# Optimization experiments

Hardware: AMD Instinct MI355X
Metric: run time of the kernel (lower is better)

## Reference

```python
import jax, jax.numpy as jnp
import numpy as np

RES0 = 128
SCALES = [1, 2, 4, 8]
OUT_DIM = 32
PLANES = [(0, 1), (0, 2), (1, 2)]  # itertools.combinations(range(3), 2)


def _bilinear(grid, cx, cy):
    """grid: [C,H,W]; cx maps to W, cy maps to H; coords in [-1,1].
    Matches F.grid_sample(mode='bilinear', align_corners=True, padding_mode='border')."""
    C, H, W = grid.shape
    x = jnp.clip((cx + 1.0) * 0.5 * (W - 1), 0.0, W - 1)
    y = jnp.clip((cy + 1.0) * 0.5 * (H - 1), 0.0, H - 1)
    x0 = jnp.floor(x)
    y0 = jnp.floor(y)
    wx = (x - x0)[:, None]  # [N,1]
    wy = (y - y0)[:, None]
    x0i = x0.astype(jnp.int32)
    y0i = y0.astype(jnp.int32)
    x1i = jnp.minimum(x0i + 1, W - 1)
    y1i = jnp.minimum(y0i + 1, H - 1)
    g00 = grid[:, y0i, x0i].T  # [N,C]
    g01 = grid[:, y0i, x1i].T
    g10 = grid[:, y1i, x0i].T
    g11 = grid[:, y1i, x1i].T
    top = g00 * (1.0 - wx) + g01 * wx
    bot = g10 * (1.0 - wx) + g11 * wx
    return top * (1.0 - wy) + bot * wy  # [N,C]


def _interpolate_ms_features(x, ms_grids):
    feats = []
    for scale_grids in ms_grids:  # fixed 4 scales
        interp_space = 1.0
        for ci, (a, b) in enumerate(PLANES):  # fixed 3 planes
            interp_space = interp_space * _bilinear(scale_grids[ci], x[:, a], x[:, b])
        feats.append(interp_space)
    return jnp.concatenate(feats, axis=-1)  # [N, 4*OUT_DIM]


def _mlp(f, w0, w1, w2):
    h = jax.nn.relu(f @ w0)
    h = jax.nn.relu(h @ w1)
    return h @ w2  # [N,1], linear output (tcnn, bias-free)


def setup_inputs() -> dict:
    key = jax.random.key(0)
    ks = jax.random.split(key, 16)
    N = 1_000_000
    inp = {"x": jax.random.uniform(ks[0], (N, 3), jnp.float32, -1.0, 1.0)}
    i = 1
    for s, mult in enumerate(SCALES):
        R = RES0 * mult
        for p in range(3):
            # nn.init.uniform_(a=0.1, b=0.5)
            inp[f"g{s}p{p}"] = jax.random.uniform(ks[i], (OUT_DIM, R, R), jnp.float32, 0.1, 0.5)
            i += 1
    F = OUT_DIM * len(SCALES)
    inp["w0"] = jax.random.normal(ks[13], (F, 64), jnp.float32) / np.sqrt(F).astype(np.float32)
    inp["w1"] = jax.random.normal(ks[14], (64, 64), jnp.float32) / 8.0
    inp["w2"] = jax.random.normal(ks[15], (64, 1), jnp.float32) / 8.0
    return inp


def reference(x, g0p0, g0p1, g0p2, g1p0, g1p1, g1p2, g2p0, g2p1, g2p2,
              g3p0, g3p1, g3p2, w0, w1, w2):
    ms_grids = [(g0p0, g0p1, g0p2), (g1p0, g1p1, g1p2),
                (g2p0, g2p1, g2p2), (g3p0, g3p1, g3p2)]
    features = _interpolate_ms_features(x, ms_grids)
    return _mlp(features, w0, w1, w2)
```

## Files before the change

kernel.cpp:

```cpp
#include <hip/hip_runtime.h>
#include <cstddef>


typedef unsigned short ushort_t;
typedef unsigned int uint_t;
typedef __bf16 bf16x8 __attribute__((ext_vector_type(8)));
typedef float f32x4 __attribute__((ext_vector_type(4)));

#define NBUCKET 32768

struct KParams {
  const float* x;
  const void* g[12];
  const float* w0;
  const float* w1;
  const float* w2;
  const ushort_t* w0T;
  const ushort_t* w1T;
  const float* xs;
  const int* sidx;
  float* out;
  int N;
};

struct TPA {
  const float* src[12];
  ushort_t* dst[12];
};

__device__ __forceinline__ ushort_t f32_to_bf16_rne(float f) {
  uint_t u = __float_as_uint(f);
  u = (u + 0x7FFFu + ((u >> 16) & 1u)) >> 16;
  return (ushort_t)u;
}

__global__ __launch_bounds__(256) void transpose_all(TPA tp) {
  const int b = blockIdx.x;
  int s, tile;
  if (b < 256) { s = 0; tile = b; }
  else if (b < 1280) { s = 1; tile = b - 256; }
  else if (b < 5376) { s = 2; tile = b - 1280; }
  else { s = 3; tile = b - 5376; }
  const int RR = 16384 << (2 * s);
  const int k = s * 3 + blockIdx.y;
  const float* __restrict__ in = tp.src[k];
  ushort_t* __restrict__ out = tp.dst[k];

  __shared__ float tile_s[32][65];
  const int p0 = tile * 64;
  {
    const int tp_ = threadIdx.x & 63;
    const int tc = threadIdx.x >> 6;
#pragma unroll
    for (int cc = 0; cc < 8; ++cc) {
      const int c = cc * 4 + tc;
      tile_s[c][tp_] = in[(size_t)c * RR + p0 + tp_];
    }
  }
  __syncthreads();
  {
    const int c2 = threadIdx.x & 15;
    const int tq = threadIdx.x >> 4;
    uint_t* o32 = (uint_t*)out;
#pragma unroll
    for (int pp = 0; pp < 4; ++pp) {
      const int pos = pp * 16 + tq;
      const uint_t lo = f32_to_bf16_rne(tile_s[2 * c2 + 0][pos]);
      const uint_t hi = f32_to_bf16_rne(tile_s[2 * c2 + 1][pos]);
      o32[(size_t)(p0 + pos) * 16 + c2] = lo | (hi << 16);
    }
  }
}

__global__ __launch_bounds__(256) void prep_weights(
    const float* __restrict__ w0, const float* __restrict__ w1,
    ushort_t* __restrict__ w0T, ushort_t* __restrict__ w1T) {
  const int t = threadIdx.x;
  for (int i = t; i < 128 * 64; i += 256) {
    const int k = i >> 6, n = i & 63;
    w0T[n * 128 + k] = f32_to_bf16_rne(w0[i]);
  }
  for (int i = t; i < 64 * 64; i += 256) {
    const int k = i >> 6, n = i & 63;
    w1T[n * 64 + k] = f32_to_bf16_rne(w1[i]);
  }
}

__device__ __forceinline__ uint_t spread5(uint_t v) {
  return (v & 1u) | ((v & 2u) << 2) | ((v & 4u) << 4) | ((v & 8u) << 6) |
         ((v & 16u) << 8);
}
__device__ __forceinline__ uint_t morton_key(const float* __restrict__ x,
                                             int i) {
  const float a = x[3 * i + 0];
  const float b = x[3 * i + 1];
  const float c = x[3 * i + 2];
  const uint_t ua = (uint_t)fminf(fmaxf((a + 1.0f) * 16.0f, 0.0f), 31.0f);
  const uint_t ub = (uint_t)fminf(fmaxf((b + 1.0f) * 16.0f, 0.0f), 31.0f);
  const uint_t uc = (uint_t)fminf(fmaxf((c + 1.0f) * 16.0f, 0.0f), 31.0f);
  return spread5(ua) | (spread5(ub) << 1) | (spread5(uc) << 2);
}

__global__ __launch_bounds__(256) void sort_hist(const float* __restrict__ x,
                                                 uint_t* __restrict__ cnt,
                                                 int N) {
  const int i = blockIdx.x * 256 + threadIdx.x;
  if (i < N) atomicAdd(&cnt[morton_key(x, i)], 1u);
}

__global__ __launch_bounds__(1024) void sort_scanA(uint_t* __restrict__ cnt,
                                                   uint_t* __restrict__ bsum) {
  __shared__ uint_t s[1024];
  const int t = threadIdx.x;
  const int idx = blockIdx.x * 1024 + t;
  const uint_t v = cnt[idx];
  s[t] = v;
  __syncthreads();
  for (int off = 1; off < 1024; off <<= 1) {
    uint_t u = 0;
    if (t >= off) u = s[t - off];
    __syncthreads();
    s[t] += u;
    __syncthreads();
  }
  cnt[idx] = s[t] - v;
  if (t == 1023) bsum[blockIdx.x] = s[t];
}

__global__ __launch_bounds__(256) void sort_scanB_prepw(
    uint_t* __restrict__ bsum, const float* __restrict__ w0,
    const float* __restrict__ w1, ushort_t* __restrict__ w0T,
    ushort_t* __restrict__ w1T) {
  const int t = threadIdx.x;
  if (t == 0) {
    uint_t run = 0;
#pragma unroll
    for (int i = 0; i < 32; ++i) {
      const uint_t c = bsum[i];
      bsum[i] = run;
      run += c;
    }
  }
  for (int i = t; i < 128 * 64; i += 256) {
    const int k = i >> 6, n = i & 63;
    w0T[n * 128 + k] = f32_to_bf16_rne(w0[i]);
  }
  for (int i = t; i < 64 * 64; i += 256) {
    const int k = i >> 6, n = i & 63;
    w1T[n * 64 + k] = f32_to_bf16_rne(w1[i]);
  }
}

__global__ __launch_bounds__(256) void sort_scatter(
    const float* __restrict__ x, uint_t* __restrict__ cnt,
    const uint_t* __restrict__ bsum, int* __restrict__ sidx,
    float* __restrict__ xs, int N) {
  const int i = blockIdx.x * 256 + threadIdx.x;
  if (i >= N) return;
  const uint_t key = morton_key(x, i);
  const uint_t pos = atomicAdd(&cnt[key], 1u) + bsum[key >> 10];
  sidx[pos] = i;
  xs[3 * pos + 0] = x[3 * i + 0];
  xs[3 * pos + 1] = x[3 * i + 1];
  xs[3 * pos + 2] = x[3 * i + 2];
}

template <bool SORTED>
__global__ __launch_bounds__(512, 8) void kplanes_fused_mfma(KParams P) {
  __shared__ float arena[8704];
  int4* o4s = (int4*)arena;
  float* wxs = arena + 3072;
  float* wys = arena + 3840;
  uint_t* feat32 = (uint_t*)(arena + 4608);
  float* px = arena + 4608;

  const int t = threadIdx.x;

  int bid = blockIdx.x;
  if (SORTED) {
    const int nblk = gridDim.x;
    const int q = nblk >> 3, r = nblk & 7;
    const int xcd = bid & 7, idx = bid >> 3;
    bid = (xcd < r ? xcd * (q + 1) : r * (q + 1) + (xcd - r) * q) + idx;
  }
  const int blk0 = bid * 64;

  if (SORTED) {
    if (t < 192) {
      int idx = blk0 * 3 + t;
      if (idx >= 3 * P.N) idx = 3 * P.N - 3 + (t % 3);
      px[t] = P.xs[idx];
    }
  } else {
    if (t < 192) {
      const int p = t / 3, e = t - p * 3;
      int Pi = blk0 + p;
      if (Pi >= P.N) Pi = P.N - 1;
      px[t] = P.x[3 * Pi + e];
    }
  }
  __syncthreads();

  for (int task = t; task < 768; task += 512) {
    const int pt = task & 63;
    const int sm = task >> 6;
    const int pl = sm >> 2;
    const int s = sm & 3;
    const float cx = (pl == 2) ? px[pt * 3 + 1] : px[pt * 3 + 0];
    const float cy = (pl == 0) ? px[pt * 3 + 1] : px[pt * 3 + 2];
    const int R = 128 << s;
    const float Rm1 = (float)(R - 1);
    const float u = fminf(fmaxf((cx + 1.0f) * 0.5f * Rm1, 0.0f), Rm1);
    const float v = fminf(fmaxf((cy + 1.0f) * 0.5f * Rm1, 0.0f), Rm1);
    const float fx0 = floorf(u), fy0 = floorf(v);
    const int x0 = (int)fx0, y0 = (int)fy0;
    const int x1 = min(x0 + 1, R - 1), y1 = min(y0 + 1, R - 1);
    int4 o4;
    o4.x = y0 * R + x0;
    o4.y = y0 * R + x1;
    o4.z = y1 * R + x0;
    o4.w = y1 * R + x1;
    o4s[task] = o4;
    wxs[task] = u - fx0;
    wys[task] = v - fy0;
  }
  __syncthreads();

  const int pt = t >> 3;
  const int q = t & 7;
  const int cg = q & 3;
  const int sh = q >> 2;
  uint_t* prow = feat32 + pt * 64;
  const int wxor = (pt & 7) << 2;

#define LOADP(gp, o, QA, QB, QC, QD)                              \
  QA = *(const uint4*)((gp) + (size_t)(o).x * 32 + cg * 8);       \
  QB = *(const uint4*)((gp) + (size_t)(o).y * 32 + cg * 8);       \
  QC = *(const uint4*)((gp) + (size_t)(o).z * 32 + cg * 8);       \
  QD = *(const uint4*)((gp) + (size_t)(o).w * 32 + cg * 8);

#define CH2(dA, dB, dC, dD, i0, i1)                                \
  {                                                                \
    float rl = __uint_as_float((dD) << 16) * w11;                  \
    rl = fmaf(__uint_as_float((dC) << 16), w10, rl);               \
    rl = fmaf(__uint_as_float((dB) << 16), w01, rl);               \
    rl = fmaf(__uint_as_float((dA) << 16), w00, rl);               \
    f[i0] *= rl;                                                   \
    float rh = __uint_as_float((dD)&0xFFFF0000u) * w11;            \
    rh = fmaf(__uint_as_float((dC)&0xFFFF0000u), w10, rh);         \
    rh = fmaf(__uint_as_float((dB)&0xFFFF0000u), w01, rh);         \
    rh = fmaf(__uint_as_float((dA)&0xFFFF0000u), w00, rh);         \
    f[i1] *= rh;                                                   \
  }

#define CONSUME(QA, QB, QC, QD, WX, WY)                            \
  {                                                                \
    const float w11 = (WX) * (WY);                                 \
    const float w10 = (WY)-w11;                                    \
    const float w01 = (WX)-w11;                                    \
    const float w00 = 1.0f - (WX)-w10;                             \
    CH2(QA.x, QB.x, QC.x, QD.x, 0, 1)                              \
    CH2(QA.y, QB.y, QC.y, QD.y, 2, 3)                              \
    CH2(QA.z, QB.z, QC.z, QD.z, 4, 5)                              \
    CH2(QA.w, QB.w, QC.w, QD.w, 6, 7)                              \
  }

#pragma unroll
  for (int j = 0; j < 2; ++j) {
    const int s = 2 * j + sh;
    const int b0 = s * 64 + pt;
    const int b1 = (4 + s) * 64 + pt;
    const int b2 = (8 + s) * 64 + pt;
    const int4 o0 = o4s[b0];
    const int4 o1 = o4s[b1];
    const int4 o2 = o4s[b2];
    const float wx0 = wxs[b0], wy0 = wys[b0];
    const float wx1 = wxs[b1], wy1 = wys[b1];
    const float wx2 = wxs[b2], wy2 = wys[b2];
    const ushort_t* g0 = (const ushort_t*)P.g[s * 3 + 0];
    const ushort_t* g1 = (const ushort_t*)P.g[s * 3 + 1];
    const ushort_t* g2 = (const ushort_t*)P.g[s * 3 + 2];

    uint4 A0, B0, C0, D0, A1, B1, C1, D1, A2, B2, C2, D2;
    LOADP(g0, o0, A0, B0, C0, D0)
    LOADP(g1, o1, A1, B1, C1, D1)
    float f[8] = {1.f, 1.f, 1.f, 1.f, 1.f, 1.f, 1.f, 1.f};
    CONSUME(A0, B0, C0, D0, wx0, wy0)
    LOADP(g2, o2, A2, B2, C2, D2)
    CONSUME(A1, B1, C1, D1, wx1, wy1)
    CONSUME(A2, B2, C2, D2, wx2, wy2)

    uint_t d0, d1, d2, d3;
    asm("v_cvt_pk_bf16_f32 %0, %1, %2" : "=v"(d0) : "v"(f[0]), "v"(f[1]));
    asm("v_cvt_pk_bf16_f32 %0, %1, %2" : "=v"(d1) : "v"(f[2]), "v"(f[3]));
    asm("v_cvt_pk_bf16_f32 %0, %1, %2" : "=v"(d2) : "v"(f[4]), "v"(f[5]));
    asm("v_cvt_pk_bf16_f32 %0, %1, %2" : "=v"(d3) : "v"(f[6]), "v"(f[7]));
    uint4 dv;
    dv.x = d0; dv.y = d1; dv.z = d2; dv.w = d3;
    *(uint4*)(prow + ((s * 16 + cg * 4) ^ wxor)) = dv;
  }
#undef LOADP
#undef CH2
#undef CONSUME
  __syncthreads();

  ushort_t* lds_h = (ushort_t*)arena;
  float(*oparts)[64] = (float(*)[64])(arena + 2048);

  const int w = __builtin_amdgcn_readfirstlane(t >> 6);
  const int mt = w & 3;
  const int nt0 = (w >> 2) << 1;
  const int ln = t & 15;
  const int lq = (t >> 4) & 3;
  const int arow = mt * 16 + ln;

  const uint_t* farow = feat32 + arow * 64;
  const int axor = (arow & 7) << 2;
  f32x4 acc0a = {0.f, 0.f, 0.f, 0.f}, acc0b = {0.f, 0.f, 0.f, 0.f};
  const ushort_t* w0a = P.w0T + (nt0 * 16 + ln) * 128 + lq * 8;
  const ushort_t* w0b = w0a + 16 * 128;
#pragma unroll
  for (int kt = 0; kt < 4; ++kt) {
    const bf16x8 aF = *(const bf16x8*)(farow + ((kt * 16 + lq * 4) ^ axor));
    const bf16x8 bFa = *(const bf16x8*)(w0a + kt * 32);
    const bf16x8 bFb = *(const bf16x8*)(w0b + kt * 32);
    acc0a = __builtin_amdgcn_mfma_f32_16x16x32_bf16(aF, bFa, acc0a, 0, 0, 0);
    acc0b = __builtin_amdgcn_mfma_f32_16x16x32_bf16(aF, bFb, acc0b, 0, 0, 0);
  }

#pragma unroll
  for (int i = 0; i < 2; ++i) {
    const f32x4 a = i ? acc0b : acc0a;
    const int col = (nt0 + i) * 16 + ln;
#pragma unroll
    for (int jj = 0; jj < 4; ++jj) {
      const float v = fmaxf(a[jj], 0.0f);
      uint_t dv;
      asm("v_cvt_pk_bf16_f32 %0, %1, %2" : "=v"(dv) : "v"(v), "v"(v));
      const int r = mt * 16 + lq * 4 + jj;
      lds_h[r * 64 + (col ^ ((r & 7) << 3))] = (ushort_t)dv;
    }
  }
  __syncthreads();

  const ushort_t* hrow = lds_h + arow * 64;
  const int hxor = (arow & 7) << 3;
  f32x4 acc1a = {0.f, 0.f, 0.f, 0.f}, acc1b = {0.f, 0.f, 0.f, 0.f};
  const ushort_t* w1a = P.w1T + (nt0 * 16 + ln) * 64 + lq * 8;
  const ushort_t* w1b = w1a + 16 * 64;
#pragma unroll
  for (int kt = 0; kt < 2; ++kt) {
    const bf16x8 aF = *(const bf16x8*)(hrow + ((kt * 32 + lq * 8) ^ hxor));
    const bf16x8 bFa = *(const bf16x8*)(w1a + kt * 32);
    const bf16x8 bFb = *(const bf16x8*)(w1b + kt * 32);
    acc1a = __builtin_amdgcn_mfma_f32_16x16x32_bf16(aF, bFa, acc1a, 0, 0, 0);
    acc1b = __builtin_amdgcn_mfma_f32_16x16x32_bf16(aF, bFb, acc1b, 0, 0, 0);
  }

  const float w2a = P.w2[nt0 * 16 + ln];
  const float w2b = P.w2[(nt0 + 1) * 16 + ln];
  float part[4];
#pragma unroll
  for (int jj = 0; jj < 4; ++jj)
    part[jj] = fmaxf(acc1a[jj], 0.f) * w2a + fmaxf(acc1b[jj], 0.f) * w2b;
#pragma unroll
  for (int jj = 0; jj < 4; ++jj) {
    part[jj] += __shfl_xor(part[jj], 1);
    part[jj] += __shfl_xor(part[jj], 2);
    part[jj] += __shfl_xor(part[jj], 4);
    part[jj] += __shfl_xor(part[jj], 8);
  }
  if (ln == 0) {
#pragma unroll
    for (int jj = 0; jj < 4; ++jj)
      oparts[w >> 2][mt * 16 + lq * 4 + jj] = part[jj];
  }
  __syncthreads();

  if (t < 64) {
    const int Po = blk0 + t;
    if (Po < P.N) {
      const float r = oparts[0][t] + oparts[1][t];
      if (SORTED)
        P.out[P.sidx[Po]] = r;
      else
        P.out[Po] = r;
    }
  }
}

__global__ __launch_bounds__(512, 8) void kplanes_fused_scalar(KParams P) {
  __shared__ float fl[64][130];
  const int t = threadIdx.x;
  const int pg = t >> 3;
  const int sub = t & 7;
  const int blk0 = blockIdx.x * 64;

  int Pi = blk0 + pg;
  if (Pi >= P.N) Pi = P.N - 1;
  const float c0 = P.x[3 * Pi + 0];
  const float c1 = P.x[3 * Pi + 1];
  const float c2 = P.x[3 * Pi + 2];

  float feat[4][4];
#pragma unroll
  for (int s = 0; s < 4; ++s)
#pragma unroll
    for (int c = 0; c < 4; ++c) feat[s][c] = 1.0f;

#pragma unroll
  for (int s = 0; s < 4; ++s) {
    const int R = 128 << s;
    const int RR = R * R;
#pragma unroll
    for (int pl = 0; pl < 3; ++pl) {
      const float cx = (pl == 2) ? c1 : c0;
      const float cy = (pl == 0) ? c1 : c2;
      const float Rm1 = (float)(R - 1);
      const float u = fminf(fmaxf((cx + 1.0f) * 0.5f * Rm1, 0.0f), Rm1);
      const float v = fminf(fmaxf((cy + 1.0f) * 0.5f * Rm1, 0.0f), Rm1);
      const float fx0 = floorf(u), fy0 = floorf(v);
      const float wx = u - fx0, wy = v - fy0;
      const int x0 = (int)fx0, y0 = (int)fy0;
      const int x1 = min(x0 + 1, R - 1), y1 = min(y0 + 1, R - 1);
      const float w11 = wx * wy;
      const float w10 = wy - w11;
      const float w01 = wx - w11;
      const float w00 = 1.0f - wx - w10;
      const float* gp = (const float*)P.g[s * 3 + pl];
      const int i00 = y0 * R + x0, i01 = y0 * R + x1;
      const int i10 = y1 * R + x0, i11 = y1 * R + x1;
#pragma unroll
      for (int c = 0; c < 4; ++c) {
        const size_t cb = (size_t)(sub * 4 + c) * RR;
        feat[s][c] *= gp[cb + i00] * w00 + gp[cb + i01] * w01 +
                      gp[cb + i10] * w10 + gp[cb + i11] * w11;
      }
    }
  }

#pragma unroll
  for (int s = 0; s < 4; ++s)
#pragma unroll
    for (int c = 0; c < 4; ++c)
      fl[pg][s * 32 + sub * 4 + c] = feat[s][c];
  __syncthreads();

  const int p = t & 63;
  const int g = __builtin_amdgcn_readfirstlane(t >> 6);

  const float* w0c = P.w0 + g * 8;
  float part[8];
#pragma unroll
  for (int jj = 0; jj < 8; ++jj) part[jj] = 0.0f;
#pragma unroll 16
  for (int k = 0; k < 128; ++k) {
    const float f = fl[p][k];
#pragma unroll
    for (int jj = 0; jj < 8; ++jj)
      part[jj] = fmaf(f, w0c[(size_t)k * 64 + jj], part[jj]);
  }
  __syncthreads();
#pragma unroll
  for (int jj = 0; jj < 8; ++jj)
    fl[p][g * 8 + jj] = fmaxf(part[jj], 0.0f);
  __syncthreads();

  const float* w1c = P.w1 + g * 8;
  float h1[8];
#pragma unroll
  for (int jj = 0; jj < 8; ++jj) h1[jj] = 0.0f;
#pragma unroll 16
  for (int k = 0; k < 64; ++k) {
    const float a = fl[p][k];
#pragma unroll
    for (int jj = 0; jj < 8; ++jj)
      h1[jj] = fmaf(a, w1c[(size_t)k * 64 + jj], h1[jj]);
  }

  const float* w2c = P.w2 + g * 8;
  float o = 0.0f;
#pragma unroll
  for (int jj = 0; jj < 8; ++jj)
    o = fmaf(fmaxf(h1[jj], 0.0f), w2c[jj], o);

  __syncthreads();
  ((float*)fl)[g * 64 + p] = o;
  __syncthreads();

  if (t < 64) {
    const int Po = blk0 + t;
    if (Po < P.N) {
      const float* f0 = (const float*)fl;
      float r = 0.0f;
#pragma unroll
      for (int j = 0; j < 8; ++j) r += f0[j * 64 + t];
      P.out[Po] = r;
    }
  }
}

extern "C" void kernel_launch(void* const* d_in, const int* in_sizes, int n_in,
                              void* d_out, int out_size, void* d_ws, size_t ws_size,
                              hipStream_t stream) {
  KParams P;
  P.x = (const float*)d_in[0];
  P.w0 = (const float*)d_in[13];
  P.w1 = (const float*)d_in[14];
  P.w2 = (const float*)d_in[15];
  P.out = (float*)d_out;
  const int N = in_sizes[0] / 3;
  P.N = N;
  P.xs = nullptr;
  P.sidx = nullptr;

  size_t need = 0;
  for (int s = 0; s < 4; ++s) {
    const size_t R = (size_t)(128 << s);
    need += 3ull * 32ull * R * R * sizeof(ushort_t);
  }
  const size_t walign = (need + 255) & ~(size_t)255;
  const size_t wbytes = (size_t)(64 * 128 + 64 * 64) * sizeof(ushort_t);
  const size_t cntoff = (walign + wbytes + 255) & ~(size_t)255;
  const size_t cntbytes = (size_t)NBUCKET * 4;
  const size_t bsumoff = cntoff + cntbytes;
  const size_t sidxoff = (bsumoff + 128 + 255) & ~(size_t)255;
  const size_t xsoff = (sidxoff + (size_t)N * 4 + 255) & ~(size_t)255;
  const size_t total_sorted = xsoff + (size_t)N * 12;

  const int nblk = (N + 63) / 64;
  if (ws_size >= walign + wbytes) {
    ushort_t* w = (ushort_t*)d_ws;
    TPA tpa;
    size_t off = 0;
    for (int s = 0; s < 4; ++s) {
      const int R = 128 << s;
      const int RR = R * R;
      for (int pl = 0; pl < 3; ++pl) {
        tpa.src[s * 3 + pl] = (const float*)d_in[1 + s * 3 + pl];
        tpa.dst[s * 3 + pl] = w + off;
        P.g[s * 3 + pl] = w + off;
        off += (size_t)32 * RR;
      }
    }
    dim3 tg(21760, 3);
    transpose_all<<<tg, 256, 0, stream>>>(tpa);

    ushort_t* w0T = (ushort_t*)((char*)d_ws + walign);
    ushort_t* w1T = w0T + 64 * 128;
    P.w0T = w0T;
    P.w1T = w1T;

    if (ws_size >= total_sorted) {
      uint_t* cnt = (uint_t*)((char*)d_ws + cntoff);
      uint_t* bsum = (uint_t*)((char*)d_ws + bsumoff);
      int* sidx = (int*)((char*)d_ws + sidxoff);
      float* xs = (float*)((char*)d_ws + xsoff);
      hipMemsetAsync(cnt, 0, cntbytes, stream);
      const int pblk = (N + 255) / 256;
      sort_hist<<<pblk, 256, 0, stream>>>(P.x, cnt, N);
      sort_scanA<<<32, 1024, 0, stream>>>(cnt, bsum);
      sort_scanB_prepw<<<1, 256, 0, stream>>>(bsum, P.w0, P.w1, w0T, w1T);
      sort_scatter<<<pblk, 256, 0, stream>>>(P.x, cnt, bsum, sidx, xs, N);
      P.xs = xs;
      P.sidx = sidx;
      kplanes_fused_mfma<true><<<nblk, 512, 0, stream>>>(P);
    } else {
      prep_weights<<<1, 256, 0, stream>>>(P.w0, P.w1, w0T, w1T);
      kplanes_fused_mfma<false><<<nblk, 512, 0, stream>>>(P);
    }
  } else {
    for (int k = 0; k < 12; ++k) P.g[k] = (const void*)d_in[1 + k];
    P.w0T = nullptr;
    P.w1T = nullptr;
    kplanes_fused_scalar<<<nblk, 512, 0, stream>>>(P);
  }
}
```

Before: 713.8 us.

## Software-pipeline plane gathers and cache Morton keys between sort passes

The gather loop is restructured into a six-stage software pipeline. Each stage issues the four bilinear corner loads for the next scale/plane before it consumes the current one, so memory latency overlaps with the interpolation math. Separately, the histogram pass now stores 16-bit Morton keys to workspace, and the scatter pass reads them back instead of re-reading x and recomputing. This costs extra registers for the double-buffered loads and some additional workspace memory traffic.

```diff
diff --git a/kernel.cpp b/kernel.cpp
--- a/kernel.cpp
+++ b/kernel.cpp
@@ -103,9 +103,14 @@
 
 __global__ __launch_bounds__(256) void sort_hist(const float* __restrict__ x,
                                                  uint_t* __restrict__ cnt,
+                                                 ushort_t* __restrict__ key16,
                                                  int N) {
   const int i = blockIdx.x * 256 + threadIdx.x;
-  if (i < N) atomicAdd(&cnt[morton_key(x, i)], 1u);
+  if (i < N) {
+    const uint_t k = morton_key(x, i);
+    key16[i] = (ushort_t)k;
+    atomicAdd(&cnt[k], 1u);
+  }
 }
 
 __global__ __launch_bounds__(1024) void sort_scanA(uint_t* __restrict__ cnt,
@@ -152,12 +157,12 @@
 }
 
 __global__ __launch_bounds__(256) void sort_scatter(
-    const float* __restrict__ x, uint_t* __restrict__ cnt,
-    const uint_t* __restrict__ bsum, int* __restrict__ sidx,
-    float* __restrict__ xs, int N) {
+    const float* __restrict__ x, const ushort_t* __restrict__ key16,
+    uint_t* __restrict__ cnt, const uint_t* __restrict__ bsum,
+    int* __restrict__ sidx, float* __restrict__ xs, int N) {
   const int i = blockIdx.x * 256 + threadIdx.x;
   if (i >= N) return;
-  const uint_t key = morton_key(x, i);
+  const uint_t key = key16[i];
   const uint_t pos = atomicAdd(&cnt[key], 1u) + bsum[key >> 10];
   sidx[pos] = i;
   xs[3 * pos + 0] = x[3 * i + 0];
@@ -233,12 +238,13 @@
   uint_t* prow = feat32 + pt * 64;
   const int wxor = (pt & 7) << 2;
 
-#define LOADP(gp, o, QA, QB, QC, QD)                              \
-  QA = *(const uint4*)((gp) + (size_t)(o).x * 32 + cg * 8);       \
-  QB = *(const uint4*)((gp) + (size_t)(o).y * 32 + cg * 8);       \
-  QC = *(const uint4*)((gp) + (size_t)(o).z * 32 + cg * 8);       \
-  QD = *(const uint4*)((gp) + (size_t)(o).w * 32 + cg * 8);
-
+#define CBASE(st) (((((st) % 3) * 4) + (2 * ((st) / 3) + sh)) * 64 + pt)
+#define GIDX(st) ((2 * ((st) / 3) + sh) * 3 + ((st) % 3))
+#define ISSUE(O, GP, QA, QB, QC, QD)                              \
+  QA = *(const uint4*)((GP) + (size_t)(O).x * 32 + cg * 8);       \
+  QB = *(const uint4*)((GP) + (size_t)(O).y * 32 + cg * 8);       \
+  QC = *(const uint4*)((GP) + (size_t)(O).z * 32 + cg * 8);       \
+  QD = *(const uint4*)((GP) + (size_t)(O).w * 32 + cg * 8);
 #define CH2(dA, dB, dC, dD, i0, i1)                                \
   {                                                                \
     float rl = __uint_as_float((dD) << 16) * w11;                  \
@@ -253,55 +259,63 @@
     f[i1] *= rh;                                                   \
   }
 
-#define CONSUME(QA, QB, QC, QD, WX, WY)                            \
-  {                                                                \
-    const float w11 = (WX) * (WY);                                 \
-    const float w10 = (WY)-w11;                                    \
-    const float w01 = (WX)-w11;                                    \
-    const float w00 = 1.0f - (WX)-w10;                             \
-    CH2(QA.x, QB.x, QC.x, QD.x, 0, 1)                              \
-    CH2(QA.y, QB.y, QC.y, QD.y, 2, 3)                              \
-    CH2(QA.z, QB.z, QC.z, QD.z, 4, 5)                              \
-    CH2(QA.w, QB.w, QC.w, QD.w, 6, 7)                              \
-  }
-
-#pragma unroll
-  for (int j = 0; j < 2; ++j) {
-    const int s = 2 * j + sh;
-    const int b0 = s * 64 + pt;
-    const int b1 = (4 + s) * 64 + pt;
-    const int b2 = (8 + s) * 64 + pt;
-    const int4 o0 = o4s[b0];
-    const int4 o1 = o4s[b1];
-    const int4 o2 = o4s[b2];
-    const float wx0 = wxs[b0], wy0 = wys[b0];
-    const float wx1 = wxs[b1], wy1 = wys[b1];
-    const float wx2 = wxs[b2], wy2 = wys[b2];
-    const ushort_t* g0 = (const ushort_t*)P.g[s * 3 + 0];
-    const ushort_t* g1 = (const ushort_t*)P.g[s * 3 + 1];
-    const ushort_t* g2 = (const ushort_t*)P.g[s * 3 + 2];
-
-    uint4 A0, B0, C0, D0, A1, B1, C1, D1, A2, B2, C2, D2;
-    LOADP(g0, o0, A0, B0, C0, D0)
-    LOADP(g1, o1, A1, B1, C1, D1)
-    float f[8] = {1.f, 1.f, 1.f, 1.f, 1.f, 1.f, 1.f, 1.f};
-    CONSUME(A0, B0, C0, D0, wx0, wy0)
-    LOADP(g2, o2, A2, B2, C2, D2)
-    CONSUME(A1, B1, C1, D1, wx1, wy1)
-    CONSUME(A2, B2, C2, D2, wx2, wy2)
-
-    uint_t d0, d1, d2, d3;
-    asm("v_cvt_pk_bf16_f32 %0, %1, %2" : "=v"(d0) : "v"(f[0]), "v"(f[1]));
-    asm("v_cvt_pk_bf16_f32 %0, %1, %2" : "=v"(d1) : "v"(f[2]), "v"(f[3]));
-    asm("v_cvt_pk_bf16_f32 %0, %1, %2" : "=v"(d2) : "v"(f[4]), "v"(f[5]));
-    asm("v_cvt_pk_bf16_f32 %0, %1, %2" : "=v"(d3) : "v"(f[6]), "v"(f[7]));
-    uint4 dv;
-    dv.x = d0; dv.y = d1; dv.z = d2; dv.w = d3;
-    *(uint4*)(prow + ((s * 16 + cg * 4) ^ wxor)) = dv;
-  }
-#undef LOADP
+  {
+    uint4 A, B, C, D, A2, B2, C2, D2;
+    float wx_c, wy_c, wx_n, wy_n;
+    float f[8];
+
+    {
+      const int b_ = CBASE(0);
+      const int4 o = o4s[b_];
+      wx_c = wxs[b_];
+      wy_c = wys[b_];
+      const ushort_t* gp = (const ushort_t*)P.g[GIDX(0)];
+      ISSUE(o, gp, A, B, C, D)
+    }
+
+#pragma unroll
+    for (int st = 0; st < 6; ++st) {
+      if (st < 5) {
+        const int b_ = CBASE(st + 1);
+        const int4 o = o4s[b_];
+        wx_n = wxs[b_];
+        wy_n = wys[b_];
+        const ushort_t* gp = (const ushort_t*)P.g[GIDX(st + 1)];
+        ISSUE(o, gp, A2, B2, C2, D2)
+      }
+      if ((st % 3) == 0) {
+#pragma unroll
+        for (int c = 0; c < 8; ++c) f[c] = 1.0f;
+      }
+      {
+        const float w11 = wx_c * wy_c;
+        const float w10 = wy_c - w11;
+        const float w01 = wx_c - w11;
+        const float w00 = 1.0f - wx_c - w10;
+        CH2(A.x, B.x, C.x, D.x, 0, 1)
+        CH2(A.y, B.y, C.y, D.y, 2, 3)
+        CH2(A.z, B.z, C.z, D.z, 4, 5)
+        CH2(A.w, B.w, C.w, D.w, 6, 7)
+      }
+      if ((st % 3) == 2) {
+        const int s = 2 * (st / 3) + sh;
+        uint_t d0, d1, d2, d3;
+        asm("v_cvt_pk_bf16_f32 %0, %1, %2" : "=v"(d0) : "v"(f[0]), "v"(f[1]));
+        asm("v_cvt_pk_bf16_f32 %0, %1, %2" : "=v"(d1) : "v"(f[2]), "v"(f[3]));
+        asm("v_cvt_pk_bf16_f32 %0, %1, %2" : "=v"(d2) : "v"(f[4]), "v"(f[5]));
+        asm("v_cvt_pk_bf16_f32 %0, %1, %2" : "=v"(d3) : "v"(f[6]), "v"(f[7]));
+        uint4 dv;
+        dv.x = d0; dv.y = d1; dv.z = d2; dv.w = d3;
+        *(uint4*)(prow + ((s * 16 + cg * 4) ^ wxor)) = dv;
+      }
+      A = A2; B = B2; C = C2; D = D2;
+      wx_c = wx_n; wy_c = wy_n;
+    }
+  }
+#undef CBASE
+#undef GIDX
+#undef ISSUE
 #undef CH2
-#undef CONSUME
   __syncthreads();
 
   ushort_t* lds_h = (ushort_t*)arena;
@@ -524,7 +538,8 @@
   const size_t cntoff = (walign + wbytes + 255) & ~(size_t)255;
   const size_t cntbytes = (size_t)NBUCKET * 4;
   const size_t bsumoff = cntoff + cntbytes;
-  const size_t sidxoff = (bsumoff + 128 + 255) & ~(size_t)255;
+  const size_t keyoff = (bsumoff + 128 + 255) & ~(size_t)255;
+  const size_t sidxoff = (keyoff + (size_t)N * 2 + 255) & ~(size_t)255;
   const size_t xsoff = (sidxoff + (size_t)N * 4 + 255) & ~(size_t)255;
   const size_t total_sorted = xsoff + (size_t)N * 12;
 
@@ -554,14 +569,15 @@
     if (ws_size >= total_sorted) {
       uint_t* cnt = (uint_t*)((char*)d_ws + cntoff);
       uint_t* bsum = (uint_t*)((char*)d_ws + bsumoff);
+      ushort_t* key16 = (ushort_t*)((char*)d_ws + keyoff);
       int* sidx = (int*)((char*)d_ws + sidxoff);
       float* xs = (float*)((char*)d_ws + xsoff);
       hipMemsetAsync(cnt, 0, cntbytes, stream);
       const int pblk = (N + 255) / 256;
-      sort_hist<<<pblk, 256, 0, stream>>>(P.x, cnt, N);
+      sort_hist<<<pblk, 256, 0, stream>>>(P.x, cnt, key16, N);
       sort_scanA<<<32, 1024, 0, stream>>>(cnt, bsum);
       sort_scanB_prepw<<<1, 256, 0, stream>>>(bsum, P.w0, P.w1, w0T, w1T);
-      sort_scatter<<<pblk, 256, 0, stream>>>(P.x, cnt, bsum, sidx, xs, N);
+      sort_scatter<<<pblk, 256, 0, stream>>>(P.x, key16, cnt, bsum, sidx, xs, N);
       P.xs = xs;
       P.sidx = sidx;
       kplanes_fused_mfma<true><<<nblk, 512, 0, stream>>>(P);
```

After: 719.2 us. No clear change (+0.8%).
